# Performance work log

Measured on AMD Instinct MI355X. Metric: run time of the kernel, lower is better.

## Reference

```python
import jax, jax.numpy as jnp
import numpy as np

D_MODEL = 2048
N_HEADS = 16
D_HEAD = 128
BATCH = 2
SEQ = 2048
INIT_STD = 0.02
N_LAYERS = 12


def setup_inputs() -> dict:
    key = jax.random.key(0)
    ks = jax.random.split(key, 5)
    attn_std = INIT_STD
    proj_std = INIT_STD / np.sqrt(2 * N_LAYERS)
    return {
        "normalized_resid_pre": jax.random.normal(ks[0], (BATCH, SEQ, D_MODEL), jnp.float32),
        "W_Q": jax.random.normal(ks[1], (N_HEADS, D_MODEL, D_HEAD), jnp.float32) * attn_std,
        "W_K": jax.random.normal(ks[2], (N_HEADS, D_MODEL, D_HEAD), jnp.float32) * attn_std,
        "W_V": jax.random.normal(ks[3], (N_HEADS, D_MODEL, D_HEAD), jnp.float32) * attn_std,
        "W_O": jax.random.normal(ks[4], (N_HEADS, D_HEAD, D_MODEL), jnp.float32) * proj_std,
        "b_Q": jnp.zeros((N_HEADS, D_HEAD), jnp.float32),
        "b_K": jnp.zeros((N_HEADS, D_HEAD), jnp.float32),
        "b_V": jnp.zeros((N_HEADS, D_HEAD), jnp.float32),
        "b_O": jnp.zeros((D_MODEL,), jnp.float32),
    }


def reference(normalized_resid_pre, W_Q, W_K, W_V, W_O, b_Q, b_K, b_V, b_O):
    x = normalized_resid_pre
    # q,k,v: [batch, posn, nheads, d_head]
    q = jnp.einsum('bsd,hde->bshe', x, W_Q) + b_Q
    k = jnp.einsum('bsd,hde->bshe', x, W_K) + b_K
    v = jnp.einsum('bsd,hde->bshe', x, W_V) + b_V
    # scores: [batch, nheads, posn_Q, posn_K]
    scores = jnp.einsum('bqhe,bkhe->bhqk', q, k) / jnp.sqrt(jnp.float32(D_HEAD))
    S = scores.shape[-1]
    causal = jnp.tril(jnp.ones((S, S), bool))
    scores = jnp.where(causal, scores, jnp.float32(-jnp.inf))
    pattern = jax.nn.softmax(scores, axis=-1)
    z = jnp.einsum('bhqk,bkhe->bqhe', pattern, v)
    attn_out = jnp.einsum('bqhe,hed->bqd', z, W_O) + b_O
    return attn_out
```

## Files before the change

kernel.cpp:

```cpp
#include <hip/hip_runtime.h>
#include <hip/hip_bf16.h>

typedef __hip_bfloat16 bf16;
typedef __attribute__((ext_vector_type(8))) short bf16x8;
typedef __attribute__((ext_vector_type(4))) short bf16x4;
typedef __attribute__((ext_vector_type(4))) float f32x4;

#define D_MODEL 2048
#define SEQ     2048
#define NH      16
#define DH      128
#define BATCH   2
#define MTOT    (BATCH*SEQ)

__device__ __forceinline__ void async_cp16(const bf16* g, bf16* l) {
    __builtin_amdgcn_global_load_lds(
        (const __attribute__((address_space(1))) void*)g,
        (__attribute__((address_space(3))) void*)l, 16, 0, 0);
}

__device__ __forceinline__ short bf16bits(float f) {
    bf16 b = __float2bfloat16(f);
    return *reinterpret_cast<short*>(&b);
}

#define GBAR() do { asm volatile("" ::: "memory"); __builtin_amdgcn_s_barrier(); \
                    asm volatile("" ::: "memory"); } while (0)

__global__ __launch_bounds__(256) void cvt_k(const float* __restrict__ in,
                                             bf16* __restrict__ out) {
    const long i = ((long)blockIdx.x * 256 + threadIdx.x) * 8;
    float4 a = *(const float4*)(in + i);
    float4 b = *(const float4*)(in + i + 4);
    __align__(16) bf16 t[8];
    t[0] = __float2bfloat16(a.x); t[1] = __float2bfloat16(a.y);
    t[2] = __float2bfloat16(a.z); t[3] = __float2bfloat16(a.w);
    t[4] = __float2bfloat16(b.x); t[5] = __float2bfloat16(b.y);
    t[6] = __float2bfloat16(b.z); t[7] = __float2bfloat16(b.w);
    *(bf16x8*)(out + i) = *(const bf16x8*)t;
}

__global__ __launch_bounds__(256) void transpose_cvt3_k(
    const float* __restrict__ in0, const float* __restrict__ in1,
    const float* __restrict__ in2,
    bf16* __restrict__ out, int R, int Cn, int mats_per_src)
{
    __shared__ float t[32][33];
    const int z = blockIdx.z;
    const int src = z / mats_per_src, mat = z % mats_per_src;
    const float* in = (src == 0) ? in0 : (src == 1) ? in1 : in2;
    const float* inm = in + (long)mat * R * Cn;
    bf16* outm = out + (long)z * R * Cn;
    const int c0 = blockIdx.x * 32, r0 = blockIdx.y * 32;
    const int tx = threadIdx.x & 31, ty = threadIdx.x >> 5;
#pragma unroll
    for (int i = 0; i < 4; ++i)
        t[ty + i*8][tx] = inm[(long)(r0 + ty + i*8) * Cn + c0 + tx];
    __syncthreads();
#pragma unroll
    for (int i = 0; i < 4; ++i)
        outm[(long)(c0 + ty + i*8) * R + r0 + tx] = __float2bfloat16(t[tx][ty + i*8]);
}

__global__ __launch_bounds__(256) void transpose_v_k(
    const bf16* __restrict__ V, bf16* __restrict__ VT)
{
    __shared__ bf16 t[32][33];
    const int bh = blockIdx.z;
    const int b = bh >> 4, h = bh & 15;
    const bf16* inm = V + (long)b*SEQ*D_MODEL + h*DH;
    bf16* outm = VT + (long)bh*DH*SEQ;
    const int r0 = blockIdx.x * 32;
    const int c0 = blockIdx.y * 32;
    const int tx = threadIdx.x & 31, ty = threadIdx.x >> 5;
#pragma unroll
    for (int i = 0; i < 4; ++i)
        t[ty + i*8][tx] = inm[(long)(r0 + ty + i*8)*D_MODEL + c0 + tx];
    __syncthreads();
#pragma unroll
    for (int i = 0; i < 4; ++i)
        outm[(long)(c0 + ty + i*8)*SEQ + r0 + tx] = t[tx][ty + i*8];
}

template <bool C_F32>
__device__ __forceinline__ void gemm128x128(
    const bf16* __restrict__ A, int lda,
    const bf16* __restrict__ Bt, int ldb,
    void* __restrict__ C, int ldc,
    const float* __restrict__ bias,
    int Kdim, int m0, int n0)
{
    __shared__ __align__(16) bf16 As[128*32];
    __shared__ __align__(16) bf16 Bs[128*32];
    const int tid  = threadIdx.x;
    const int wave = tid >> 6, lane = tid & 63;
    const int lr = lane & 15, lq = lane >> 4;
    const int wrow = wave >> 1, wcol = wave & 1;
    const int sr = lane >> 2, sk = (lane & 3) * 8;

    const f32x4 zero4 = {0.f, 0.f, 0.f, 0.f};
    f32x4 acc[4][4];
#pragma unroll
    for (int i = 0; i < 4; ++i)
#pragma unroll
        for (int j = 0; j < 4; ++j) acc[i][j] = zero4;

    for (int k0 = 0; k0 < Kdim; k0 += 32) {
#pragma unroll
        for (int c = 0; c < 2; ++c) {
            const int r = wave*32 + c*16;
            async_cp16(A  + (long)(m0 + r + sr)*lda + k0 + sk, As + r*32);
            async_cp16(Bt + (long)(n0 + r + sr)*ldb + k0 + sk, Bs + r*32);
        }
        __syncthreads();
        bf16x8 af[4], bfr[4];
#pragma unroll
        for (int i = 0; i < 4; ++i)
            af[i] = *(const bf16x8*)(As + (wrow*64 + i*16 + lr)*32 + lq*8);
#pragma unroll
        for (int j = 0; j < 4; ++j)
            bfr[j] = *(const bf16x8*)(Bs + (wcol*64 + j*16 + lr)*32 + lq*8);
#pragma unroll
        for (int i = 0; i < 4; ++i)
#pragma unroll
            for (int j = 0; j < 4; ++j)
                acc[i][j] = __builtin_amdgcn_mfma_f32_16x16x32_bf16(af[i], bfr[j], acc[i][j], 0, 0, 0);
        __syncthreads();
    }
#pragma unroll
    for (int j = 0; j < 4; ++j) {
        const int col = n0 + wcol*64 + j*16 + lr;
        const float bv = bias[col];
#pragma unroll
        for (int i = 0; i < 4; ++i) {
            const int row = m0 + wrow*64 + i*16 + lq*4;
#pragma unroll
            for (int r = 0; r < 4; ++r) {
                const float v = acc[i][j][r] + bv;
                if constexpr (C_F32) ((float*)C)[(long)(row + r)*ldc + col] = v;
                else ((bf16*)C)[(long)(row + r)*ldc + col] = __float2bfloat16(v);
            }
        }
    }
}

__global__ __launch_bounds__(256) void out_gemm_k(
    const bf16* __restrict__ Z, const bf16* __restrict__ WOT,
    const float* __restrict__ bO, float* __restrict__ Out)
{
    gemm128x128<true>(Z, D_MODEL, WOT, D_MODEL, Out, D_MODEL, bO, D_MODEL,
                      (int)blockIdx.x*128, (int)blockIdx.y*128);
}

__global__ __launch_bounds__(512, 2) void qkv_gemm256_k(
    const bf16* __restrict__ A, const bf16* __restrict__ Bt,
    const float* __restrict__ bQ, const float* __restrict__ bK, const float* __restrict__ bV,
    bf16* __restrict__ Qo, bf16* __restrict__ Ko, bf16* __restrict__ Vo)
{
    __shared__ __align__(16) bf16 lds[65536];
    bf16* As = lds;
    bf16* Bs = lds + 32768;

    const int m0 = blockIdx.x * 256;
    const int n0 = blockIdx.y * 256;
    const int tid = threadIdx.x, wave = tid >> 6, lane = tid & 63;
    const int wm = wave >> 2, wn = wave & 3;
    const int lr = lane & 15, lq = lane >> 4;
    const int sph = (lr >> 1) & 3;

    const int s_r  = lane >> 2;
    const int s_sl = lane & 3;

    auto stageA = [&](int t, int kh) {
        const int k = t*64 + kh*32;
        bf16* u = As + (((t & 1)*2 + kh) << 13);
#pragma unroll
        for (int i = 0; i < 2; ++i) {
            const int c = wave*2 + i;
            const int r = c*16 + s_r;
            async_cp16(A + (long)(m0 + r)*D_MODEL + k + ((s_sl ^ ((r >> 1) & 3)) * 8),
                       u + c*512);
        }
    };
    auto stageB = [&](int t, int kh) {
        const int k = t*64 + kh*32;
        bf16* u = Bs + (((t & 1)*2 + kh) << 13);
#pragma unroll
        for (int i = 0; i < 2; ++i) {
            const int c = wave*2 + i;
            const int r = c*16 + s_r;
            async_cp16(Bt + (long)(n0 + r)*D_MODEL + k + ((s_sl ^ ((r >> 1) & 3)) * 8),
                       u + c*512);
        }
    };
    auto rdA = [&](int t, int kh, int fm) -> bf16x8 {
        const int r = wm*128 + fm*16 + lr;
        return *(const bf16x8*)(As + (((t & 1)*2 + kh) << 13) + r*32 + ((lq ^ sph) * 8));
    };
    auto rdB = [&](int t, int kh, int fn) -> bf16x8 {
        const int r = wn*64 + fn*16 + lr;
        return *(const bf16x8*)(Bs + (((t & 1)*2 + kh) << 13) + r*32 + ((lq ^ sph) * 8));
    };

    const f32x4 zero4 = {0.f, 0.f, 0.f, 0.f};
    f32x4 acc[8][4];
#pragma unroll
    for (int i = 0; i < 8; ++i)
#pragma unroll
        for (int j = 0; j < 4; ++j) acc[i][j] = zero4;

    const int NT = D_MODEL / 64;

    stageA(0, 0); stageB(0, 0);
    stageA(0, 1); stageB(0, 1);
    stageA(1, 0); stageB(1, 0);
    asm volatile("s_waitcnt vmcnt(4)" ::: "memory");
    GBAR();

    for (int t = 0; t < NT; ++t) {
        bf16x8 aF[4], bF[4];

#pragma unroll
        for (int j = 0; j < 4; ++j) aF[j] = rdA(t, 0, j);
#pragma unroll
        for (int j = 0; j < 4; ++j) bF[j] = rdB(t, 0, j);
        if (t + 1 < NT) stageA(t + 1, 1);
        GBAR();
        __builtin_amdgcn_s_setprio(1);
#pragma unroll
        for (int j = 0; j < 4; ++j)
#pragma unroll
            for (int fn = 0; fn < 4; ++fn)
                acc[j][fn] = __builtin_amdgcn_mfma_f32_16x16x32_bf16(aF[j], bF[fn], acc[j][fn], 0, 0, 0);
        __builtin_amdgcn_s_setprio(0);
        GBAR();

#pragma unroll
        for (int j = 0; j < 4; ++j) aF[j] = rdA(t, 0, 4 + j);
        if (t + 1 < NT) stageB(t + 1, 1);
        GBAR();
        __builtin_amdgcn_s_setprio(1);
#pragma unroll
        for (int j = 0; j < 4; ++j)
#pragma unroll
            for (int fn = 0; fn < 4; ++fn)
                acc[4 + j][fn] = __builtin_amdgcn_mfma_f32_16x16x32_bf16(aF[j], bF[fn], acc[4 + j][fn], 0, 0, 0);
        __builtin_amdgcn_s_setprio(0);
        GBAR();

#pragma unroll
        for (int j = 0; j < 4; ++j) aF[j] = rdA(t, 1, j);
#pragma unroll
        for (int j = 0; j < 4; ++j) bF[j] = rdB(t, 1, j);
        if (t + 2 < NT) stageA(t + 2, 0);
        GBAR();
        __builtin_amdgcn_s_setprio(1);
#pragma unroll
        for (int j = 0; j < 4; ++j)
#pragma unroll
            for (int fn = 0; fn < 4; ++fn)
                acc[j][fn] = __builtin_amdgcn_mfma_f32_16x16x32_bf16(aF[j], bF[fn], acc[j][fn], 0, 0, 0);
        __builtin_amdgcn_s_setprio(0);
        GBAR();

#pragma unroll
        for (int j = 0; j < 4; ++j) aF[j] = rdA(t, 1, 4 + j);
        if (t + 2 < NT) stageB(t + 2, 0);
        GBAR();
        __builtin_amdgcn_s_setprio(1);
#pragma unroll
        for (int j = 0; j < 4; ++j)
#pragma unroll
            for (int fn = 0; fn < 4; ++fn)
                acc[4 + j][fn] = __builtin_amdgcn_mfma_f32_16x16x32_bf16(aF[j], bF[fn], acc[4 + j][fn], 0, 0, 0);
        __builtin_amdgcn_s_setprio(0);
        if (t < NT - 2) asm volatile("s_waitcnt vmcnt(4)" ::: "memory");
        else            asm volatile("s_waitcnt vmcnt(0)" ::: "memory");
        GBAR();
    }

    const int gc0 = n0 + wn*64;
    const int sel = gc0 >> 11;
    bf16* C        = (sel == 0) ? Qo : (sel == 1) ? Ko : Vo;
    const float* bs = (sel == 0) ? bQ : (sel == 1) ? bK : bV;
#pragma unroll
    for (int fn = 0; fn < 4; ++fn) {
        const int dcol = (gc0 + fn*16 + lr) & 2047;
        const float bv = bs[dcol];
#pragma unroll
        for (int fm = 0; fm < 8; ++fm) {
            const int row = m0 + wm*128 + fm*16 + lq*4;
#pragma unroll
            for (int rr = 0; rr < 4; ++rr)
                C[(long)(row + rr)*D_MODEL + dcol] = __float2bfloat16(acc[fm][fn][rr] + bv);
        }
    }
}

__global__ __launch_bounds__(512) void flash_k(
    const bf16* __restrict__ Q, const bf16* __restrict__ K,
    const bf16* __restrict__ VT, bf16* __restrict__ Z)
{
    __shared__ __align__(16) bf16 Ks[64*128];
    __shared__ __align__(16) bf16 Vts[128*64];
    __shared__ __align__(16) bf16 Ps[128*72];

    const int qt = (int)(gridDim.x - 1) - (int)blockIdx.x;
    const int bh = blockIdx.y;
    const int b  = bh >> 4, h = bh & 15;
    const long base = (long)b*SEQ*D_MODEL + h*DH;
    const bf16* Qb  = Q + base;
    const bf16* Kb  = K + base;
    const bf16* VTb = VT + (long)bh*DH*SEQ;
    bf16* Zb = Z + base;
    const int q0 = qt*128;
    const int tid = threadIdx.x, wave = tid >> 6, lane = tid & 63;
    const int lr = lane & 15, lq = lane >> 4;
    const int rx = lr & 7;

    const int ks_key_off = lane >> 4;
    const int ks_slot    = lane & 15;
    const int vt_row_off = lane >> 3;
    const int vt_slot    = lane & 7;

    bf16x8 aq[4];
#pragma unroll
    for (int ks = 0; ks < 4; ++ks)
        aq[ks] = *(const bf16x8*)(Qb + (long)(q0 + wave*16 + lr)*D_MODEL + ks*32 + lq*8);

    const f32x4 zero4 = {0.f, 0.f, 0.f, 0.f};
    f32x4 o_acc[8];
#pragma unroll
    for (int jf = 0; jf < 8; ++jf) o_acc[jf] = zero4;
    float m_run = -1e30f, l_run = 0.f;

    const float scale = 0.08838834764831845f;
    const int NT = 2*qt + 2;

    for (int kt = 0; kt < NT; ++kt) {
        const int k0 = kt*64;
        __syncthreads();
#pragma unroll
        for (int c2 = 0; c2 < 2; ++c2) {
            const int c = wave*2 + c2;
            const int key = c*4 + ks_key_off;
            async_cp16(Kb + (long)(k0 + key)*D_MODEL + ((ks_slot ^ (key & 7)) * 8),
                       Ks + c*512);
            const int f = c*8 + vt_row_off;
            async_cp16(VTb + (long)f*SEQ + k0 + ((vt_slot ^ (f & 7)) * 8),
                       Vts + c*512);
        }
        __syncthreads();

        const int rel_hi = q0 + wave*16 + 15 - k0;
        if (rel_hi >= 0) {
            f32x4 sc[4];
#pragma unroll
            for (int mt = 0; mt < 4; ++mt) sc[mt] = zero4;
            __builtin_amdgcn_s_setprio(1);
#pragma unroll
            for (int mt = 0; mt < 4; ++mt)
#pragma unroll
                for (int ks = 0; ks < 4; ++ks) {
                    bf16x8 bk = *(const bf16x8*)(Ks + (mt*16 + lr)*128 + (((ks*4 + lq) ^ rx) * 8));
                    sc[mt] = __builtin_amdgcn_mfma_f32_16x16x32_bf16(bk, aq[ks], sc[mt], 0, 0, 0);
                }
            __builtin_amdgcn_s_setprio(0);

            if (rel_hi < 78) {
                const int rel = q0 + wave*16 + lr - k0;
#pragma unroll
                for (int mt = 0; mt < 4; ++mt)
#pragma unroll
                    for (int r = 0; r < 4; ++r)
                        if (mt*16 + lq*4 + r > rel) sc[mt][r] = -1e30f;
            }

            float mx = sc[0][0];
#pragma unroll
            for (int mt = 0; mt < 4; ++mt)
#pragma unroll
                for (int r = 0; r < 4; ++r) mx = fmaxf(mx, sc[mt][r]);
            mx = fmaxf(mx, __shfl_xor(mx, 16, 64));
            mx = fmaxf(mx, __shfl_xor(mx, 32, 64));
            mx *= scale;

            if (!__all(mx - m_run <= 8.0f)) {
                const float mn = fmaxf(m_run, mx);
                const float al = __expf(m_run - mn);
                l_run *= al;
#pragma unroll
                for (int jf = 0; jf < 8; ++jf)
#pragma unroll
                    for (int r = 0; r < 4; ++r) o_acc[jf][r] *= al;
                m_run = mn;
            }

            float rs = 0.f;
#pragma unroll
            for (int mt = 0; mt < 4; ++mt)
#pragma unroll
                for (int r = 0; r < 4; ++r) {
                    const float p = __expf(fmaf(sc[mt][r], scale, -m_run));
                    sc[mt][r] = p;
                    rs += p;
                }
            rs += __shfl_xor(rs, 16, 64);
            rs += __shfl_xor(rs, 32, 64);
            l_run += rs;

#pragma unroll
            for (int mt = 0; mt < 4; ++mt) {
                bf16x4 pk;
#pragma unroll
                for (int r = 0; r < 4; ++r) pk[r] = bf16bits(sc[mt][r]);
                *(bf16x4*)(Ps + (wave*16 + lr)*72 + mt*16 + lq*4) = pk;
            }

            bf16x8 pb0 = *(const bf16x8*)(Ps + (wave*16 + lr)*72 + lq*8);
            bf16x8 pb1 = *(const bf16x8*)(Ps + (wave*16 + lr)*72 + 32 + lq*8);

            __builtin_amdgcn_s_setprio(1);
#pragma unroll
            for (int jf = 0; jf < 8; ++jf) {
                const int f = jf*16 + lr;
                bf16x8 av0 = *(const bf16x8*)(Vts + f*64 + ((lq ^ rx) * 8));
                bf16x8 av1 = *(const bf16x8*)(Vts + f*64 + (((4 + lq) ^ rx) * 8));
                o_acc[jf] = __builtin_amdgcn_mfma_f32_16x16x32_bf16(av0, pb0, o_acc[jf], 0, 0, 0);
                o_acc[jf] = __builtin_amdgcn_mfma_f32_16x16x32_bf16(av1, pb1, o_acc[jf], 0, 0, 0);
            }
            __builtin_amdgcn_s_setprio(0);
        }
    }

    const float inv = 1.f / l_run;
    const long zrow = (long)(q0 + wave*16 + lr) * D_MODEL;
#pragma unroll
    for (int jf = 0; jf < 8; ++jf) {
        bf16x4 pk;
#pragma unroll
        for (int r = 0; r < 4; ++r) pk[r] = bf16bits(o_acc[jf][r] * inv);
        *(bf16x4*)(Zb + zrow + jf*16 + lq*4) = pk;
    }
}

extern "C" void kernel_launch(void* const* d_in, const int* in_sizes, int n_in,
                              void* d_out, int out_size, void* d_ws, size_t ws_size,
                              hipStream_t stream) {
    const float* X  = (const float*)d_in[0];
    const float* WQ = (const float*)d_in[1];
    const float* WK = (const float*)d_in[2];
    const float* WV = (const float*)d_in[3];
    const float* WO = (const float*)d_in[4];
    const float* bQ = (const float*)d_in[5];
    const float* bK = (const float*)d_in[6];
    const float* bV = (const float*)d_in[7];
    const float* bO = (const float*)d_in[8];
    float* out = (float*)d_out;

    bf16* ws = (bf16*)d_ws;
    const long WSZ = (long)NH*DH*D_MODEL;
    const long MSZ = (long)MTOT*D_MODEL;
    bf16* Xb  = ws;
    bf16* WT3 = Xb + MSZ;
    bf16* WOT = WT3 + 3*WSZ;
    bf16* Qb  = WOT + WSZ;
    bf16* Kb  = Qb + MSZ;
    bf16* Vb  = Kb + MSZ;
    bf16* Zb  = Xb;
    bf16* VT  = WT3;

    cvt_k<<<MSZ/(256*8), 256, 0, stream>>>(X, Xb);
    transpose_cvt3_k<<<dim3(DH/32, D_MODEL/32, 3*NH), 256, 0, stream>>>(
        WQ, WK, WV, WT3, D_MODEL, DH, NH);
    transpose_cvt3_k<<<dim3(D_MODEL/32, D_MODEL/32, 1), 256, 0, stream>>>(
        WO, WO, WO, WOT, D_MODEL, D_MODEL, 1);

    qkv_gemm256_k<<<dim3(MTOT/256, 3*D_MODEL/256), 512, 0, stream>>>(
        Xb, WT3, bQ, bK, bV, Qb, Kb, Vb);
    transpose_v_k<<<dim3(SEQ/32, DH/32, BATCH*NH), 256, 0, stream>>>(Vb, VT);
    flash_k<<<dim3(SEQ/128, BATCH*NH), 512, 0, stream>>>(Qb, Kb, VT, Zb);
    out_gemm_k<<<dim3(MTOT/128, D_MODEL/128), 256, 0, stream>>>(Zb, WOT, bO, out);
}
```

Baseline: 410.6 us.

## Halve QKV GEMM LDS buffering, raise occupancy, and swizzle block order

The QKV projection GEMM drops from double-buffered to single-buffered LDS (64KB to 32KB per block), raises the launch bound to 4 blocks per CU, and adds a 1D grid with a swizzled block-to-tile mapping for L2 locality. Loads for the second k-half are issued during compute on the first half, with a full vmcnt(0) wait each half-step. The aim is more resident waves to hide latency in place of deep software prefetch. The cost is less load/compute overlap per block and tighter register pressure from 64 accumulators under a 4-block bound, which risks spills.

```diff
diff --git a/kernel.cpp b/kernel.cpp
--- a/kernel.cpp
+++ b/kernel.cpp
@@ -152,17 +152,20 @@
                       (int)blockIdx.x*128, (int)blockIdx.y*128);
 }
 
-__global__ __launch_bounds__(512, 2) void qkv_gemm256_k(
+__global__ __launch_bounds__(512, 4) void qkv_gemm256_k(
     const bf16* __restrict__ A, const bf16* __restrict__ Bt,
     const float* __restrict__ bQ, const float* __restrict__ bK, const float* __restrict__ bV,
     bf16* __restrict__ Qo, bf16* __restrict__ Ko, bf16* __restrict__ Vo)
 {
-    __shared__ __align__(16) bf16 lds[65536];
+    __shared__ __align__(16) bf16 lds[32768];
     bf16* As = lds;
-    bf16* Bs = lds + 32768;
-
-    const int m0 = blockIdx.x * 256;
-    const int n0 = blockIdx.y * 256;
+    bf16* Bs = lds + 16384;
+
+    const int lin = blockIdx.x;
+    const int swz = (lin & 7) * 48 + (lin >> 3);
+    const int m0 = (swz & 15) * 256;
+    const int n0 = (swz >> 4) * 256;
+
     const int tid = threadIdx.x, wave = tid >> 6, lane = tid & 63;
     const int wm = wave >> 2, wn = wave & 3;
     const int lr = lane & 15, lq = lane >> 4;
@@ -173,7 +176,7 @@
 
     auto stageA = [&](int t, int kh) {
         const int k = t*64 + kh*32;
-        bf16* u = As + (((t & 1)*2 + kh) << 13);
+        bf16* u = As + (kh << 13);
 #pragma unroll
         for (int i = 0; i < 2; ++i) {
             const int c = wave*2 + i;
@@ -184,7 +187,7 @@
     };
     auto stageB = [&](int t, int kh) {
         const int k = t*64 + kh*32;
-        bf16* u = Bs + (((t & 1)*2 + kh) << 13);
+        bf16* u = Bs + (kh << 13);
 #pragma unroll
         for (int i = 0; i < 2; ++i) {
             const int c = wave*2 + i;
@@ -193,13 +196,13 @@
                        u + c*512);
         }
     };
-    auto rdA = [&](int t, int kh, int fm) -> bf16x8 {
+    auto rdA = [&](int kh, int fm) -> bf16x8 {
         const int r = wm*128 + fm*16 + lr;
-        return *(const bf16x8*)(As + (((t & 1)*2 + kh) << 13) + r*32 + ((lq ^ sph) * 8));
+        return *(const bf16x8*)(As + (kh << 13) + r*32 + ((lq ^ sph) * 8));
     };
-    auto rdB = [&](int t, int kh, int fn) -> bf16x8 {
+    auto rdB = [&](int kh, int fn) -> bf16x8 {
         const int r = wn*64 + fn*16 + lr;
-        return *(const bf16x8*)(Bs + (((t & 1)*2 + kh) << 13) + r*32 + ((lq ^ sph) * 8));
+        return *(const bf16x8*)(Bs + (kh << 13) + r*32 + ((lq ^ sph) * 8));
     };
 
     const f32x4 zero4 = {0.f, 0.f, 0.f, 0.f};
@@ -212,19 +215,17 @@
     const int NT = D_MODEL / 64;
 
     stageA(0, 0); stageB(0, 0);
-    stageA(0, 1); stageB(0, 1);
-    stageA(1, 0); stageB(1, 0);
-    asm volatile("s_waitcnt vmcnt(4)" ::: "memory");
+    asm volatile("s_waitcnt vmcnt(0)" ::: "memory");
     GBAR();
 
     for (int t = 0; t < NT; ++t) {
         bf16x8 aF[4], bF[4];
 
 #pragma unroll
-        for (int j = 0; j < 4; ++j) aF[j] = rdA(t, 0, j);
-#pragma unroll
-        for (int j = 0; j < 4; ++j) bF[j] = rdB(t, 0, j);
-        if (t + 1 < NT) stageA(t + 1, 1);
+        for (int j = 0; j < 4; ++j) aF[j] = rdA(0, j);
+#pragma unroll
+        for (int j = 0; j < 4; ++j) bF[j] = rdB(0, j);
+        stageA(t, 1); stageB(t, 1);
         GBAR();
         __builtin_amdgcn_s_setprio(1);
 #pragma unroll
@@ -236,8 +237,7 @@
         GBAR();
 
 #pragma unroll
-        for (int j = 0; j < 4; ++j) aF[j] = rdA(t, 0, 4 + j);
-        if (t + 1 < NT) stageB(t + 1, 1);
+        for (int j = 0; j < 4; ++j) aF[j] = rdA(0, 4 + j);
         GBAR();
         __builtin_amdgcn_s_setprio(1);
 #pragma unroll
@@ -246,13 +246,14 @@
             for (int fn = 0; fn < 4; ++fn)
                 acc[4 + j][fn] = __builtin_amdgcn_mfma_f32_16x16x32_bf16(aF[j], bF[fn], acc[4 + j][fn], 0, 0, 0);
         __builtin_amdgcn_s_setprio(0);
-        GBAR();
-
-#pragma unroll
-        for (int j = 0; j < 4; ++j) aF[j] = rdA(t, 1, j);
-#pragma unroll
-        for (int j = 0; j < 4; ++j) bF[j] = rdB(t, 1, j);
-        if (t + 2 < NT) stageA(t + 2, 0);
+        asm volatile("s_waitcnt vmcnt(0)" ::: "memory");
+        GBAR();
+
+#pragma unroll
+        for (int j = 0; j < 4; ++j) aF[j] = rdA(1, j);
+#pragma unroll
+        for (int j = 0; j < 4; ++j) bF[j] = rdB(1, j);
+        if (t + 1 < NT) { stageA(t + 1, 0); stageB(t + 1, 0); }
         GBAR();
         __builtin_amdgcn_s_setprio(1);
 #pragma unroll
@@ -264,8 +265,7 @@
         GBAR();
 
 #pragma unroll
-        for (int j = 0; j < 4; ++j) aF[j] = rdA(t, 1, 4 + j);
-        if (t + 2 < NT) stageB(t + 2, 0);
+        for (int j = 0; j < 4; ++j) aF[j] = rdA(1, 4 + j);
         GBAR();
         __builtin_amdgcn_s_setprio(1);
 #pragma unroll
@@ -274,8 +274,7 @@
             for (int fn = 0; fn < 4; ++fn)
                 acc[4 + j][fn] = __builtin_amdgcn_mfma_f32_16x16x32_bf16(aF[j], bF[fn], acc[4 + j][fn], 0, 0, 0);
         __builtin_amdgcn_s_setprio(0);
-        if (t < NT - 2) asm volatile("s_waitcnt vmcnt(4)" ::: "memory");
-        else            asm volatile("s_waitcnt vmcnt(0)" ::: "memory");
+        asm volatile("s_waitcnt vmcnt(0)" ::: "memory");
         GBAR();
     }
 
@@ -476,7 +475,7 @@
     transpose_cvt3_k<<<dim3(D_MODEL/32, D_MODEL/32, 1), 256, 0, stream>>>(
         WO, WO, WO, WOT, D_MODEL, D_MODEL, 1);
 
-    qkv_gemm256_k<<<dim3(MTOT/256, 3*D_MODEL/256), 512, 0, stream>>>(
+    qkv_gemm256_k<<<dim3((MTOT/256)*(3*D_MODEL/256)), 512, 0, stream>>>(
         Xb, WT3, bQ, bK, bV, Qb, Kb, Vb);
     transpose_v_k<<<dim3(SEQ/32, DH/32, BATCH*NH), 256, 0, stream>>>(Vb, VT);
     flash_k<<<dim3(SEQ/128, BATCH*NH), 512, 0, stream>>>(Qb, Kb, VT, Zb);
```

After: 1.324 ms. 3.22x slower.
